# Kernel optimization log

Hardware: AMD Instinct MI355X
Metric: run time of the kernel (lower is better)

The kernel has to match this reference:

```python
import jax, jax.numpy as jnp
import numpy as np

BETA = 0.25  # commitment_beta from CodebookDecoder default


def setup_inputs() -> dict:
    key = jax.random.key(0)
    k1, k2, k3 = jax.random.split(key, 3)
    Q, B, K, D = 2048, 40000, 2048, 512
    return {
        "query_emb": jax.random.normal(k1, (Q, D), dtype=jnp.float32),
        "entity_emb": jax.random.normal(k2, (B, D), dtype=jnp.float32),
        "codebook": jax.random.normal(k3, (K, D), dtype=jnp.float32),
    }


def _quantize(x, codebook):
    # Nearest-neighbor lookup. torch.norm(x[:,None]-cb[None]) argmin is
    # equivalent to argmin of squared distance, expanded to avoid the
    x2 = jnp.sum(x * x, axis=1, keepdims=True)            # (B, 1)
    c2 = jnp.sum(codebook * codebook, axis=1)             # (K,)
    d2 = x2 - 2.0 * (x @ codebook.T) + c2[None, :]        # (B, K)
    idx = jnp.argmin(d2, axis=1)                          # (B,)
    quant = codebook[idx]                                 # (B, D) gather
    # vq_loss = mse(quant.detach(), x) + beta * mse(quant, x.detach())
    vq_loss = jnp.mean((jax.lax.stop_gradient(quant) - x) ** 2) \
        + BETA * jnp.mean((quant - jax.lax.stop_gradient(x)) ** 2)
    return quant, idx, vq_loss


def reference(query_emb, entity_emb, codebook):
    quant, idx, vq_loss = _quantize(entity_emb, codebook)
    score = query_emb @ quant.T                           # (Q, B)
    return score, vq_loss, idx
```

## Files before the change

kernel.cpp:

```cpp
#include <hip/hip_runtime.h>
#include <stdint.h>

#define Q    2048
#define NB   40000
#define NK   2048
#define ND   512
#define SCORE_SIZE (Q * NB)

typedef __bf16 bf16;
typedef bf16  bf16x8 __attribute__((ext_vector_type(8)));
typedef float f32x4  __attribute__((ext_vector_type(4)));

__device__ __forceinline__ unsigned short f2bf_rne(float f) {
    unsigned int u = __float_as_uint(f);
    u += 0x7FFFu + ((u >> 16) & 1u);
    return (unsigned short)(u >> 16);
}

__device__ __forceinline__ void gl2lds16(const void* g, void* l) {
    __builtin_amdgcn_global_load_lds(
        (const __attribute__((address_space(1))) void*)g,
        (__attribute__((address_space(3))) void*)l, 16, 0, 0);
}

__global__ __launch_bounds__(256) void c2_kernel(const float* __restrict__ cb,
                                                 float* __restrict__ c2) {
    int wave = threadIdx.x >> 6, lane = threadIdx.x & 63;
    int row  = blockIdx.x * 4 + wave;
    const float4* p = (const float4*)(cb + (size_t)row * ND);
    float4 a = p[lane];
    float4 b = p[lane + 64];
    float s = a.x*a.x + a.y*a.y + a.z*a.z + a.w*a.w
            + b.x*b.x + b.y*b.y + b.z*b.z + b.w*b.w;
    #pragma unroll
    for (int off = 32; off; off >>= 1) s += __shfl_down(s, off);
    if (lane == 0) c2[row] = s;
}

__global__ __launch_bounds__(256) void cvt_bf16_kernel(const float* __restrict__ src,
                                                       unsigned short* __restrict__ dst) {
    int i = (blockIdx.x * 256 + threadIdx.x) * 4;
    float4 v = *(const float4*)(src + i);
    uint2 u;
    u.x = (unsigned int)f2bf_rne(v.x) | ((unsigned int)f2bf_rne(v.y) << 16);
    u.y = (unsigned int)f2bf_rne(v.z) | ((unsigned int)f2bf_rne(v.w) << 16);
    *(uint2*)(dst + i) = u;
}

__device__ __forceinline__ void top2_insert(float& v1, int& i1, float& v2, int& i2,
                                            float w, int j) {
    if (w < v1 || (w == v1 && j < i1)) { v2 = v1; i2 = i1; v1 = w; i1 = j; }
    else if (w < v2 || (w == v2 && j < i2)) { v2 = w; i2 = j; }
}

template<bool PRE>
__global__ __launch_bounds__(256) void dist_mfma_kernel(
        const float* __restrict__ entf, const unsigned short* __restrict__ ehi,
        const unsigned short* __restrict__ chi,
        const float* __restrict__ c2g, float4* __restrict__ partial) {
    __shared__ unsigned short Es[128 * 64];
    __shared__ unsigned short Cs[128 * 64];
    int tid = threadIdx.x;
    int b0 = blockIdx.x * 128;
    int k0 = blockIdx.y * 128;
    int lane = tid & 63, wave = tid >> 6;
    int wm = wave >> 1, wn = wave & 1;
    int lr = lane & 15, quad = lane >> 4;

    f32x4 acc[4][4] = {};

    for (int kt = 0; kt < ND; kt += 64) {
        __syncthreads();
        #pragma unroll
        for (int j = 0; j < 4; ++j) {
            int q = j * 256 + tid;
            int r = q >> 3;
            int cs = (q & 7) ^ (r & 7);
            gl2lds16(chi + (size_t)(k0 + r) * ND + kt + cs * 8,
                     Cs + (size_t)(j * 256 + wave * 64) * 8);
            int br = b0 + r; br = br < NB ? br : NB - 1;
            if (PRE) {
                gl2lds16(ehi + (size_t)br * ND + kt + cs * 8,
                         Es + (size_t)(j * 256 + wave * 64) * 8);
            } else {
                const float* s = entf + (size_t)br * ND + kt + cs * 8;
                float4 a = *(const float4*)s;
                float4 b = *(const float4*)(s + 4);
                uint4 hp;
                hp.x = (unsigned int)f2bf_rne(a.x) | ((unsigned int)f2bf_rne(a.y) << 16);
                hp.y = (unsigned int)f2bf_rne(a.z) | ((unsigned int)f2bf_rne(a.w) << 16);
                hp.z = (unsigned int)f2bf_rne(b.x) | ((unsigned int)f2bf_rne(b.y) << 16);
                hp.w = (unsigned int)f2bf_rne(b.z) | ((unsigned int)f2bf_rne(b.w) << 16);
                *(uint4*)(Es + q * 8) = hp;
            }
        }
        __syncthreads();
        #pragma unroll
        for (int kq = 0; kq < 2; ++kq) {
            bf16x8 af[4], bfr[4];
            #pragma unroll
            for (int mi = 0; mi < 4; ++mi) {
                int r = wm * 64 + mi * 16 + lr;
                int ch = (kq * 4 + quad) ^ (lr & 7);
                af[mi] = *(const bf16x8*)(Es + (r * 8 + ch) * 8);
            }
            #pragma unroll
            for (int ni = 0; ni < 4; ++ni) {
                int r = wn * 64 + ni * 16 + lr;
                int ch = (kq * 4 + quad) ^ (lr & 7);
                bfr[ni] = *(const bf16x8*)(Cs + (r * 8 + ch) * 8);
            }
            #pragma unroll
            for (int mi = 0; mi < 4; ++mi)
                #pragma unroll
                for (int ni = 0; ni < 4; ++ni)
                    acc[mi][ni] = __builtin_amdgcn_mfma_f32_16x16x32_bf16(
                        af[mi], bfr[ni], acc[mi][ni], 0, 0, 0);
        }
    }

    float c2v[4];
    #pragma unroll
    for (int ni = 0; ni < 4; ++ni) c2v[ni] = c2g[k0 + wn * 64 + ni * 16 + lr];

    #pragma unroll
    for (int mi = 0; mi < 4; ++mi) {
        #pragma unroll
        for (int rr = 0; rr < 4; ++rr) {
            float v1 = 3.4e38f, v2 = 3.4e38f;
            int i1 = 0x7FFFFFFF, i2 = 0x7FFFFFFF;
            #pragma unroll
            for (int ni = 0; ni < 4; ++ni) {
                float w = c2v[ni] - 2.0f * acc[mi][ni][rr];
                top2_insert(v1, i1, v2, i2, w, k0 + wn * 64 + ni * 16 + lr);
            }
            #pragma unroll
            for (int off = 1; off < 16; off <<= 1) {
                float ov1 = __shfl_xor(v1, off); int oi1 = __shfl_xor(i1, off);
                float ov2 = __shfl_xor(v2, off); int oi2 = __shfl_xor(i2, off);
                top2_insert(v1, i1, v2, i2, ov1, oi1);
                top2_insert(v1, i1, v2, i2, ov2, oi2);
            }
            int b = b0 + wm * 64 + mi * 16 + quad * 4 + rr;
            if (lr == 0 && b < NB)
                partial[(size_t)(blockIdx.y * 2 + wn) * NB + b] =
                    make_float4(v1, __int_as_float(i1), v2, __int_as_float(i2));
        }
    }
}

__global__ __launch_bounds__(256) void cand_merge_kernel(
        const float4* __restrict__ partial, int* __restrict__ cand) {
    int b = blockIdx.x * 256 + threadIdx.x;
    if (b >= NB) return;
    float tv[8]; int ti[8];
    #pragma unroll
    for (int s = 0; s < 8; ++s) { tv[s] = 3.4e38f; ti[s] = 0x7FFFFFFF; }
    for (int g = 0; g < 32; ++g) {
        float4 p = partial[(size_t)g * NB + b];
        float pv[2] = {p.x, p.z};
        int   pi[2] = {__float_as_int(p.y), __float_as_int(p.w)};
        #pragma unroll
        for (int t = 0; t < 2; ++t) {
            float w = pv[t]; int j = pi[t];
            #pragma unroll
            for (int s = 0; s < 8; ++s) {
                if (w < tv[s] || (w == tv[s] && j < ti[s])) {
                    float tmpv = tv[s]; int tmpi = ti[s];
                    tv[s] = w; ti[s] = j; w = tmpv; j = tmpi;
                }
            }
        }
    }
    #pragma unroll
    for (int s = 0; s < 8; ++s) cand[(size_t)b * 8 + s] = ti[s];
}

__global__ __launch_bounds__(512) void rescore_kernel(
        const float* __restrict__ ent, const float* __restrict__ cb,
        const float* __restrict__ c2g, const int* __restrict__ cand,
        unsigned short* __restrict__ quantb, float* __restrict__ out_idx,
        float* __restrict__ acc) {
    int b = blockIdx.x;
    int wave = threadIdx.x >> 6, lane = threadIdx.x & 63;
    int k = cand[(size_t)b * 8 + wave];
    const float4* xp = (const float4*)(ent + (size_t)b * ND);
    const float4* cp = (const float4*)(cb + (size_t)k * ND);
    float4 x0 = xp[lane * 2], x1 = xp[lane * 2 + 1];
    float4 c0 = cp[lane * 2], c1 = cp[lane * 2 + 1];
    float s = x0.x*c0.x + x0.y*c0.y + x0.z*c0.z + x0.w*c0.w
            + x1.x*c1.x + x1.y*c1.y + x1.z*c1.z + x1.w*c1.w;
    #pragma unroll
    for (int off = 32; off; off >>= 1) s += __shfl_down(s, off);
    __shared__ float vws[8];
    __shared__ int   kws[8];
    __shared__ int   win;
    if (lane == 0) { vws[wave] = c2g[k] - 2.0f * s; kws[wave] = k; }
    __syncthreads();
    if (threadIdx.x == 0) {
        float bv = vws[0]; int bk = kws[0], bw = 0;
        #pragma unroll
        for (int w = 1; w < 8; ++w) {
            if (vws[w] < bv || (vws[w] == bv && kws[w] < bk)) {
                bv = vws[w]; bk = kws[w]; bw = w;
            }
        }
        win = bw;
        out_idx[b] = (float)bk;
    }
    __syncthreads();
    if (wave == win) {
        uint4 qp;
        qp.x = (unsigned int)f2bf_rne(c0.x) | ((unsigned int)f2bf_rne(c0.y) << 16);
        qp.y = (unsigned int)f2bf_rne(c0.z) | ((unsigned int)f2bf_rne(c0.w) << 16);
        qp.z = (unsigned int)f2bf_rne(c1.x) | ((unsigned int)f2bf_rne(c1.y) << 16);
        qp.w = (unsigned int)f2bf_rne(c1.z) | ((unsigned int)f2bf_rne(c1.w) << 16);
        *(uint4*)(quantb + (size_t)b * ND + lane * 8) = qp;
        float d0 = c0.x - x0.x, d1 = c0.y - x0.y, d2 = c0.z - x0.z, d3 = c0.w - x0.w;
        float d4 = c1.x - x1.x, d5 = c1.y - x1.y, d6 = c1.z - x1.z, d7 = c1.w - x1.w;
        float l = d0*d0 + d1*d1 + d2*d2 + d3*d3 + d4*d4 + d5*d5 + d6*d6 + d7*d7;
        #pragma unroll
        for (int off = 32; off; off >>= 1) l += __shfl_down(l, off);
        if (lane == 0) atomicAdd(acc, l);
    }
}

__global__ void vq_final_kernel(const float* __restrict__ acc, float* __restrict__ out) {
    out[0] = 1.25f * acc[0] / (float)(NB * ND);
}

__global__ __launch_bounds__(256) void score_kernel(
        const unsigned short* __restrict__ Aq, const unsigned short* __restrict__ Bq,
        float* __restrict__ C) {
    __shared__ unsigned short As[128 * 64];
    __shared__ unsigned short Bs[128 * 64];
    int tid = threadIdx.x;
    int n0 = blockIdx.x * 128;
    int m0 = blockIdx.y * 128;
    int lane = tid & 63, wave = tid >> 6;
    int wm = wave >> 1, wn = wave & 1;
    int lr = lane & 15, quad = lane >> 4;

    f32x4 acc[4][4] = {};

    for (int kt = 0; kt < ND; kt += 64) {
        __syncthreads();
        #pragma unroll
        for (int j = 0; j < 4; ++j) {
            int q = j * 256 + tid;
            int r = q >> 3;
            int cs = (q & 7) ^ (r & 7);
            gl2lds16(Aq + (size_t)(m0 + r) * ND + kt + cs * 8,
                     As + (size_t)(j * 256 + wave * 64) * 8);
            int nr = n0 + r; nr = nr < NB ? nr : NB - 1;
            gl2lds16(Bq + (size_t)nr * ND + kt + cs * 8,
                     Bs + (size_t)(j * 256 + wave * 64) * 8);
        }
        __syncthreads();
        #pragma unroll
        for (int kq = 0; kq < 2; ++kq) {
            bf16x8 af[4], bfr[4];
            #pragma unroll
            for (int mi = 0; mi < 4; ++mi) {
                int r = wm * 64 + mi * 16 + lr;
                int ch = (kq * 4 + quad) ^ (lr & 7);
                af[mi] = *(const bf16x8*)(As + (r * 8 + ch) * 8);
            }
            #pragma unroll
            for (int ni = 0; ni < 4; ++ni) {
                int r = wn * 64 + ni * 16 + lr;
                int ch = (kq * 4 + quad) ^ (lr & 7);
                bfr[ni] = *(const bf16x8*)(Bs + (r * 8 + ch) * 8);
            }
            #pragma unroll
            for (int mi = 0; mi < 4; ++mi)
                #pragma unroll
                for (int ni = 0; ni < 4; ++ni)
                    acc[mi][ni] = __builtin_amdgcn_mfma_f32_16x16x32_bf16(
                        af[mi], bfr[ni], acc[mi][ni], 0, 0, 0);
        }
    }

    #pragma unroll
    for (int mi = 0; mi < 4; ++mi) {
        #pragma unroll
        for (int ni = 0; ni < 4; ++ni) {
            int col = n0 + wn * 64 + ni * 16 + lr;
            if (col < NB) {
                #pragma unroll
                for (int r = 0; r < 4; ++r) {
                    int row = m0 + wm * 64 + mi * 16 + quad * 4 + r;
                    C[(size_t)row * NB + col] = acc[mi][ni][r];
                }
            }
        }
    }
}

extern "C" void kernel_launch(void* const* d_in, const int* in_sizes, int n_in,
                              void* d_out, int out_size, void* d_ws, size_t ws_size,
                              hipStream_t stream) {
    const float* qry = (const float*)d_in[0];
    const float* ent = (const float*)d_in[1];
    const float* cb  = (const float*)d_in[2];
    float* out = (float*)d_out;

    char* ws = (char*)d_ws;
    const bool pre = ws_size >= 100ull * 1024 * 1024;

    float4*         partial = (float4*)(ws);
    unsigned short* quantb  = (unsigned short*)(ws);
    size_t off = 40960000;
    unsigned short* ehi = nullptr;
    if (pre) { ehi = (unsigned short*)(ws + off); off += 40960000; }
    unsigned short* chi = (unsigned short*)(ws + off); off += 2097152;
    unsigned short* qb  = (unsigned short*)(ws + off); off += 2097152;
    int*            cand= (int*)(ws + off);            off += 1280000;
    float*          c2  = (float*)(ws + off);          off += 8192;
    float*          acc = (float*)(ws + off);          off += 4;

    hipMemsetAsync(acc, 0, sizeof(float), stream);

    c2_kernel<<<NK / 4, 256, 0, stream>>>(cb, c2);
    cvt_bf16_kernel<<<NK * ND / 1024, 256, 0, stream>>>(cb, chi);
    cvt_bf16_kernel<<<Q * ND / 1024, 256, 0, stream>>>(qry, qb);
    if (pre) {
        cvt_bf16_kernel<<<NB * ND / 1024, 256, 0, stream>>>(ent, ehi);
        dist_mfma_kernel<true><<<dim3(313, 16), 256, 0, stream>>>(
            ent, ehi, chi, c2, partial);
    } else {
        dist_mfma_kernel<false><<<dim3(313, 16), 256, 0, stream>>>(
            ent, nullptr, chi, c2, partial);
    }
    cand_merge_kernel<<<(NB + 255) / 256, 256, 0, stream>>>(partial, cand);
    rescore_kernel<<<NB, 512, 0, stream>>>(ent, cb, c2, cand, quantb,
                                           out + SCORE_SIZE + 1, acc);
    vq_final_kernel<<<1, 1, 0, stream>>>(acc, out + SCORE_SIZE);
    score_kernel<<<dim3(313, 16), 256, 0, stream>>>(qb, quantb, out);
}
```

Before: 1.956 ms.

## Double-buffer LDS tiles and remap block IDs across XCDs in GEMM kernels

Both the distance and score MFMA kernels now use two LDS buffers, so the next K-slice is issued before computing on the current one, with one barrier per step instead of two. Launches change from a 2D grid to a 1D grid of 5008 blocks, and the block ID is remapped so consecutive tiles on each of the 8 XCDs share the same column band, which is meant to improve L2 reuse. The cost is doubled LDS per block (64KB), which may lower occupancy.

```diff
diff --git a/kernel.cpp b/kernel.cpp
--- a/kernel.cpp
+++ b/kernel.cpp
@@ -53,70 +53,99 @@
     else if (w < v2 || (w == v2 && j < i2)) { v2 = w; i2 = j; }
 }
 
+__device__ __forceinline__ void mfma_tile(const unsigned short* __restrict__ Ab,
+                                          const unsigned short* __restrict__ Bb,
+                                          f32x4 (&acc)[4][4],
+                                          int wm, int wn, int lr, int quad) {
+    #pragma unroll
+    for (int kq = 0; kq < 2; ++kq) {
+        bf16x8 af[4], bfr[4];
+        #pragma unroll
+        for (int mi = 0; mi < 4; ++mi) {
+            int r = wm * 64 + mi * 16 + lr;
+            int ch = (kq * 4 + quad) ^ (lr & 7);
+            af[mi] = *(const bf16x8*)(Ab + ((size_t)r * 8 + ch) * 8);
+        }
+        #pragma unroll
+        for (int ni = 0; ni < 4; ++ni) {
+            int r = wn * 64 + ni * 16 + lr;
+            int ch = (kq * 4 + quad) ^ (lr & 7);
+            bfr[ni] = *(const bf16x8*)(Bb + ((size_t)r * 8 + ch) * 8);
+        }
+        #pragma unroll
+        for (int mi = 0; mi < 4; ++mi)
+            #pragma unroll
+            for (int ni = 0; ni < 4; ++ni)
+                acc[mi][ni] = __builtin_amdgcn_mfma_f32_16x16x32_bf16(
+                    af[mi], bfr[ni], acc[mi][ni], 0, 0, 0);
+    }
+}
+
+__device__ __forceinline__ void tile_coords(int bid, int& fast16, int& slow313) {
+    int wg = (bid & 7) * 626 + (bid >> 3);
+    fast16  = wg & 15;
+    slow313 = wg >> 4;
+}
+
+template<bool PRE>
+__device__ __forceinline__ void stage_dist(
+        const float* __restrict__ entf, const unsigned short* __restrict__ ehi,
+        const unsigned short* __restrict__ chi,
+        unsigned short* Eb, unsigned short* Cb,
+        int b0, int k0, int kt, int tid, int wave) {
+    #pragma unroll
+    for (int j = 0; j < 4; ++j) {
+        int q = j * 256 + tid;
+        int r = q >> 3;
+        int cs = (q & 7) ^ (r & 7);
+        gl2lds16(chi + (size_t)(k0 + r) * ND + kt + cs * 8,
+                 Cb + (size_t)(j * 256 + wave * 64) * 8);
+        int br = b0 + r; br = br < NB ? br : NB - 1;
+        if (PRE) {
+            gl2lds16(ehi + (size_t)br * ND + kt + cs * 8,
+                     Eb + (size_t)(j * 256 + wave * 64) * 8);
+        } else {
+            const float* s = entf + (size_t)br * ND + kt + cs * 8;
+            float4 a = *(const float4*)s;
+            float4 b = *(const float4*)(s + 4);
+            uint4 hp;
+            hp.x = (unsigned int)f2bf_rne(a.x) | ((unsigned int)f2bf_rne(a.y) << 16);
+            hp.y = (unsigned int)f2bf_rne(a.z) | ((unsigned int)f2bf_rne(a.w) << 16);
+            hp.z = (unsigned int)f2bf_rne(b.x) | ((unsigned int)f2bf_rne(b.y) << 16);
+            hp.w = (unsigned int)f2bf_rne(b.z) | ((unsigned int)f2bf_rne(b.w) << 16);
+            *(uint4*)(Eb + (size_t)q * 8) = hp;
+        }
+    }
+}
+
 template<bool PRE>
 __global__ __launch_bounds__(256) void dist_mfma_kernel(
         const float* __restrict__ entf, const unsigned short* __restrict__ ehi,
         const unsigned short* __restrict__ chi,
         const float* __restrict__ c2g, float4* __restrict__ partial) {
-    __shared__ unsigned short Es[128 * 64];
-    __shared__ unsigned short Cs[128 * 64];
+    __shared__ unsigned short Es[2][128 * 64];
+    __shared__ unsigned short Cs[2][128 * 64];
     int tid = threadIdx.x;
-    int b0 = blockIdx.x * 128;
-    int k0 = blockIdx.y * 128;
+    int by, bx;
+    tile_coords(blockIdx.x, by, bx);
+    int b0 = bx * 128;
+    int k0 = by * 128;
     int lane = tid & 63, wave = tid >> 6;
     int wm = wave >> 1, wn = wave & 1;
     int lr = lane & 15, quad = lane >> 4;
 
     f32x4 acc[4][4] = {};
 
-    for (int kt = 0; kt < ND; kt += 64) {
+    stage_dist<PRE>(entf, ehi, chi, Es[0], Cs[0], b0, k0, 0, tid, wave);
+    __syncthreads();
+
+    #pragma unroll
+    for (int t = 0; t < 8; ++t) {
+        if (t < 7)
+            stage_dist<PRE>(entf, ehi, chi, Es[(t + 1) & 1], Cs[(t + 1) & 1],
+                            b0, k0, (t + 1) * 64, tid, wave);
+        mfma_tile(Es[t & 1], Cs[t & 1], acc, wm, wn, lr, quad);
         __syncthreads();
-        #pragma unroll
-        for (int j = 0; j < 4; ++j) {
-            int q = j * 256 + tid;
-            int r = q >> 3;
-            int cs = (q & 7) ^ (r & 7);
-            gl2lds16(chi + (size_t)(k0 + r) * ND + kt + cs * 8,
-                     Cs + (size_t)(j * 256 + wave * 64) * 8);
-            int br = b0 + r; br = br < NB ? br : NB - 1;
-            if (PRE) {
-                gl2lds16(ehi + (size_t)br * ND + kt + cs * 8,
-                         Es + (size_t)(j * 256 + wave * 64) * 8);
-            } else {
-                const float* s = entf + (size_t)br * ND + kt + cs * 8;
-                float4 a = *(const float4*)s;
-                float4 b = *(const float4*)(s + 4);
-                uint4 hp;
-                hp.x = (unsigned int)f2bf_rne(a.x) | ((unsigned int)f2bf_rne(a.y) << 16);
-                hp.y = (unsigned int)f2bf_rne(a.z) | ((unsigned int)f2bf_rne(a.w) << 16);
-                hp.z = (unsigned int)f2bf_rne(b.x) | ((unsigned int)f2bf_rne(b.y) << 16);
-                hp.w = (unsigned int)f2bf_rne(b.z) | ((unsigned int)f2bf_rne(b.w) << 16);
-                *(uint4*)(Es + q * 8) = hp;
-            }
-        }
-        __syncthreads();
-        #pragma unroll
-        for (int kq = 0; kq < 2; ++kq) {
-            bf16x8 af[4], bfr[4];
-            #pragma unroll
-            for (int mi = 0; mi < 4; ++mi) {
-                int r = wm * 64 + mi * 16 + lr;
-                int ch = (kq * 4 + quad) ^ (lr & 7);
-                af[mi] = *(const bf16x8*)(Es + (r * 8 + ch) * 8);
-            }
-            #pragma unroll
-            for (int ni = 0; ni < 4; ++ni) {
-                int r = wn * 64 + ni * 16 + lr;
-                int ch = (kq * 4 + quad) ^ (lr & 7);
-                bfr[ni] = *(const bf16x8*)(Cs + (r * 8 + ch) * 8);
-            }
-            #pragma unroll
-            for (int mi = 0; mi < 4; ++mi)
-                #pragma unroll
-                for (int ni = 0; ni < 4; ++ni)
-                    acc[mi][ni] = __builtin_amdgcn_mfma_f32_16x16x32_bf16(
-                        af[mi], bfr[ni], acc[mi][ni], 0, 0, 0);
-        }
     }
 
     float c2v[4];
@@ -143,7 +172,7 @@
             }
             int b = b0 + wm * 64 + mi * 16 + quad * 4 + rr;
             if (lr == 0 && b < NB)
-                partial[(size_t)(blockIdx.y * 2 + wn) * NB + b] =
+                partial[(size_t)(by * 2 + wn) * NB + b] =
                     make_float4(v1, __int_as_float(i1), v2, __int_as_float(i2));
         }
     }
@@ -229,56 +258,49 @@
     out[0] = 1.25f * acc[0] / (float)(NB * ND);
 }
 
+__device__ __forceinline__ void stage_score(
+        const unsigned short* __restrict__ Aq, const unsigned short* __restrict__ Bq,
+        unsigned short* Ab, unsigned short* Bb,
+        int m0, int n0, int kt, int tid, int wave) {
+    #pragma unroll
+    for (int j = 0; j < 4; ++j) {
+        int q = j * 256 + tid;
+        int r = q >> 3;
+        int cs = (q & 7) ^ (r & 7);
+        gl2lds16(Aq + (size_t)(m0 + r) * ND + kt + cs * 8,
+                 Ab + (size_t)(j * 256 + wave * 64) * 8);
+        int nr = n0 + r; nr = nr < NB ? nr : NB - 1;
+        gl2lds16(Bq + (size_t)nr * ND + kt + cs * 8,
+                 Bb + (size_t)(j * 256 + wave * 64) * 8);
+    }
+}
+
 __global__ __launch_bounds__(256) void score_kernel(
         const unsigned short* __restrict__ Aq, const unsigned short* __restrict__ Bq,
         float* __restrict__ C) {
-    __shared__ unsigned short As[128 * 64];
-    __shared__ unsigned short Bs[128 * 64];
+    __shared__ unsigned short As[2][128 * 64];
+    __shared__ unsigned short Bs[2][128 * 64];
     int tid = threadIdx.x;
-    int n0 = blockIdx.x * 128;
-    int m0 = blockIdx.y * 128;
+    int bm, bn;
+    tile_coords(blockIdx.x, bm, bn);
+    int m0 = bm * 128;
+    int n0 = bn * 128;
     int lane = tid & 63, wave = tid >> 6;
     int wm = wave >> 1, wn = wave & 1;
     int lr = lane & 15, quad = lane >> 4;
 
     f32x4 acc[4][4] = {};
 
-    for (int kt = 0; kt < ND; kt += 64) {
+    stage_score(Aq, Bq, As[0], Bs[0], m0, n0, 0, tid, wave);
+    __syncthreads();
+
+    #pragma unroll
+    for (int t = 0; t < 8; ++t) {
+        if (t < 7)
+            stage_score(Aq, Bq, As[(t + 1) & 1], Bs[(t + 1) & 1],
+                        m0, n0, (t + 1) * 64, tid, wave);
+        mfma_tile(As[t & 1], Bs[t & 1], acc, wm, wn, lr, quad);
         __syncthreads();
-        #pragma unroll
-        for (int j = 0; j < 4; ++j) {
-            int q = j * 256 + tid;
-            int r = q >> 3;
-            int cs = (q & 7) ^ (r & 7);
-            gl2lds16(Aq + (size_t)(m0 + r) * ND + kt + cs * 8,
-                     As + (size_t)(j * 256 + wave * 64) * 8);
-            int nr = n0 + r; nr = nr < NB ? nr : NB - 1;
-            gl2lds16(Bq + (size_t)nr * ND + kt + cs * 8,
-                     Bs + (size_t)(j * 256 + wave * 64) * 8);
-        }
-        __syncthreads();
-        #pragma unroll
-        for (int kq = 0; kq < 2; ++kq) {
-            bf16x8 af[4], bfr[4];
-            #pragma unroll
-            for (int mi = 0; mi < 4; ++mi) {
-                int r = wm * 64 + mi * 16 + lr;
-                int ch = (kq * 4 + quad) ^ (lr & 7);
-                af[mi] = *(const bf16x8*)(As + (r * 8 + ch) * 8);
-            }
-            #pragma unroll
-            for (int ni = 0; ni < 4; ++ni) {
-                int r = wn * 64 + ni * 16 + lr;
-                int ch = (kq * 4 + quad) ^ (lr & 7);
-                bfr[ni] = *(const bf16x8*)(Bs + (r * 8 + ch) * 8);
-            }
-            #pragma unroll
-            for (int mi = 0; mi < 4; ++mi)
-                #pragma unroll
-                for (int ni = 0; ni < 4; ++ni)
-                    acc[mi][ni] = __builtin_amdgcn_mfma_f32_16x16x32_bf16(
-                        af[mi], bfr[ni], acc[mi][ni], 0, 0, 0);
-        }
     }
 
     #pragma unroll
@@ -326,15 +348,15 @@
     cvt_bf16_kernel<<<Q * ND / 1024, 256, 0, stream>>>(qry, qb);
     if (pre) {
         cvt_bf16_kernel<<<NB * ND / 1024, 256, 0, stream>>>(ent, ehi);
-        dist_mfma_kernel<true><<<dim3(313, 16), 256, 0, stream>>>(
+        dist_mfma_kernel<true><<<5008, 256, 0, stream>>>(
             ent, ehi, chi, c2, partial);
     } else {
-        dist_mfma_kernel<false><<<dim3(313, 16), 256, 0, stream>>>(
+        dist_mfma_kernel<false><<<5008, 256, 0, stream>>>(
             ent, nullptr, chi, c2, partial);
     }
     cand_merge_kernel<<<(NB + 255) / 256, 256, 0, stream>>>(partial, cand);
     rescore_kernel<<<NB, 512, 0, stream>>>(ent, cb, c2, cand, quantb,
                                            out + SCORE_SIZE + 1, acc);
     vq_final_kernel<<<1, 1, 0, stream>>>(acc, out + SCORE_SIZE);
-    score_kernel<<<dim3(313, 16), 256, 0, stream>>>(qb, quantb, out);
-}
+    score_kernel<<<5008, 256, 0, stream>>>(qb, quantb, out);
+}
```

After: 1.974 ms. Within noise of the previous version (+0.9%).
